# Kernel tuning notes

Hardware: AMD Instinct MI355X
Metric: run time of the kernel (lower is better)

The kernel has to match this reference:

```python
import jax, jax.numpy as jnp
import numpy as np

NUM_HEADS = 16
NUM_KV_HEADS = 4
HEAD_DIM = 64
ROPE_BASE = 10000.0


def _rope(x, pos0):
    # x: [b, s, n, h_d]; interleaved-pair RoPE (torchtune RotaryPositionalEmbeddings)
    b, s, n, hd = x.shape
    half = hd // 2
    inv_freq = 1.0 / (ROPE_BASE ** (jnp.arange(0, hd, 2, dtype=jnp.float32) / hd))  # [half]
    t = jnp.arange(s, dtype=jnp.float32) + pos0                                      # [s]
    freqs = t[:, None] * inv_freq[None, :]                                           # [s, half]
    cos = jnp.cos(freqs)[None, :, None, :].astype(x.dtype)
    sin = jnp.sin(freqs)[None, :, None, :].astype(x.dtype)
    xr = x.reshape(b, s, n, half, 2)
    x1, x2 = xr[..., 0], xr[..., 1]
    o1 = x1 * cos - x2 * sin
    o2 = x1 * sin + x2 * cos
    return jnp.stack([o1, o2], axis=-1).reshape(b, s, n, hd)


def setup_inputs() -> dict:
    key = jax.random.key(0)
    k1, k2, k3 = jax.random.split(key, 3)
    b, s, d = 2, 2048, 1024
    qkv_dim = (NUM_HEADS + 2 * NUM_KV_HEADS) * HEAD_DIM  # 1536
    x = jax.random.normal(k1, (b, s, d), dtype=jnp.float32)
    Wqkv = jax.random.normal(k2, (d, qkv_dim), dtype=jnp.float32) * (d ** -0.5)
    Wo = jax.random.normal(k3, (d, d), dtype=jnp.float32) * (d ** -0.5)
    return {"x": x, "Wqkv": Wqkv, "Wo": Wo, "curr_pos": 0}


def reference(x, Wqkv, Wo, curr_pos):
    b, s, d = x.shape
    n_h, n_kv, hd = NUM_HEADS, NUM_KV_HEADS, HEAD_DIM
    q_per_kv = n_h // n_kv
    total_qkv = q_per_kv + 2

    # fused QKV projection then split per kv group
    qkv = (x @ Wqkv).reshape(b, s, n_kv, total_qkv, hd)
    q = qkv[:, :, :, :q_per_kv]            # [b, s, n_kv, q_per_kv, hd]
    k = qkv[:, :, :, q_per_kv:q_per_kv + 1]  # [b, s, n_kv, 1, hd]
    v = qkv[:, :, :, q_per_kv + 1:]          # [b, s, n_kv, 1, hd]

    # GQA expand k/v to match query heads, then flatten heads
    k = jnp.broadcast_to(k, (b, s, n_kv, q_per_kv, hd))
    v = jnp.broadcast_to(v, (b, s, n_kv, q_per_kv, hd))
    q = q.reshape(b, s, n_h, hd)
    k = k.reshape(b, s, n_h, hd)
    v = v.reshape(b, s, n_h, hd)

    # RoPE on q and k
    q = _rope(q, curr_pos)
    k = _rope(k, curr_pos)

    # causal SDPA (kv_cache is None -> is_causal=True, mask=None, dropout=0)
    scale = 1.0 / jnp.sqrt(jnp.asarray(hd, dtype=x.dtype))
    scores = jnp.einsum('bqhd,bkhd->bhqk', q, k) * scale  # [b, n_h, s, s]
    causal = jnp.tril(jnp.ones((s, s), dtype=bool))
    scores = jnp.where(causal[None, None], scores, jnp.finfo(scores.dtype).min)
    attn = jax.nn.softmax(scores, axis=-1)
    out = jnp.einsum('bhqk,bkhd->bqhd', attn, v).reshape(b, s, n_h * hd)
    return out @ Wo
```

## Files before the change

### kernel.cpp

```cpp
#include <hip/hip_runtime.h>
#include <hip/hip_bf16.h>

typedef __attribute__((ext_vector_type(8))) short bf16x8;
typedef __attribute__((ext_vector_type(4))) short bf16x4;
typedef __attribute__((ext_vector_type(4))) float f32x4;
typedef unsigned short u16;
typedef unsigned int u32;

#define NH 16
#define NKV 4
#define HD 64
#define BB 2
#define SS 2048
#define DD 1024
#define QKVD 1536

#define QSCALE 0.18033688011112f
#define MBIAS  -12.0f

template<bool B> struct BoolC { static constexpr bool value = B; };
template<int V>  struct IntC  { static constexpr int value = V; };

__device__ __forceinline__ u16 f2b(float f){
  __hip_bfloat16 h = __float2bfloat16(f);
  u16 u; __builtin_memcpy(&u, &h, 2); return u;
}
__device__ __forceinline__ float b2f(u32 u){
  u <<= 16; float f; __builtin_memcpy(&f, &u, 4); return f;
}
__device__ __forceinline__ float exp2fast(float x){
#if __has_builtin(__builtin_amdgcn_exp2f)
  return __builtin_amdgcn_exp2f(x);
#else
  return exp2f(x);
#endif
}

__device__ __forceinline__ void gload16(const void* g, void* l){
  __builtin_amdgcn_global_load_lds((const __attribute__((address_space(1))) void*)g,
                                   (__attribute__((address_space(3))) void*)l, 16, 0, 0);
}

__device__ __forceinline__ f32x4 mfma16(bf16x4 a, bf16x4 b, f32x4 c){
#if __has_builtin(__builtin_amdgcn_mfma_f32_16x16x16bf16_1k)
  return __builtin_amdgcn_mfma_f32_16x16x16bf16_1k(a, b, c, 0, 0, 0);
#else
  asm volatile("v_mfma_f32_16x16x16_bf16 %0, %1, %2, %0" : "+v"(c) : "v"(a), "v"(b));
  return c;
#endif
}

__global__ __launch_bounds__(256) void prep1(const float* __restrict__ x,
                                             u16* __restrict__ Xb,
                                             const float* __restrict__ Wqkv,
                                             u16* __restrict__ WqkvT,
                                             const float* __restrict__ Wo,
                                             u16* __restrict__ WoT){
  __shared__ u16 tile[64][65];
  const int bid = blockIdx.x;
  if (bid < 4096){
    int idx = (bid * 256 + threadIdx.x) * 4;
    float4 v = *(const float4*)(x + idx);
    u32 lo = (u32)f2b(v.x) | ((u32)f2b(v.y) << 16);
    u32 hi = (u32)f2b(v.z) | ((u32)f2b(v.w) << 16);
    *(uint2*)(Xb + idx) = make_uint2(lo, hi);
    return;
  }
  const float* in; u16* outT; int K, N, n0, k0;
  if (bid < 4480){
    int id = bid - 4096; in = Wqkv; outT = WqkvT; K = 1024; N = 1536;
    n0 = (id % 24) * 64; k0 = (id / 24) * 64;
  } else {
    int id = bid - 4480; in = Wo; outT = WoT; K = 1024; N = 1024;
    n0 = (id % 16) * 64; k0 = (id / 16) * 64;
  }
  int cr = threadIdx.x >> 6, cc = threadIdx.x & 63;
#pragma unroll
  for (int rr = 0; rr < 16; rr++){
    int row = rr * 4 + cr;
    tile[row][cc] = f2b(in[(size_t)(k0 + row) * N + n0 + cc]);
  }
  __syncthreads();
#pragma unroll
  for (int rr = 0; rr < 16; rr++){
    int row = rr * 4 + cr;
    outT[(size_t)(n0 + row) * K + k0 + cc] = tile[cc][row];
  }
}

template<int TN, typename OT>
__global__ __launch_bounds__(256) void gemm_db(const __hip_bfloat16* __restrict__ A,
                                               const __hip_bfloat16* __restrict__ BT,
                                               OT* __restrict__ C,
                                               int M, int N, int K){
  constexpr int NW = TN / 32;
  constexpr int ABYTES = 128 * 128;
  constexpr int BBYTES = TN * 128;
  __shared__ __align__(16) char smem[2][ABYTES + BBYTES];
  const int ntn = N / TN;
  int bid = blockIdx.x;
  const int cpx = gridDim.x >> 3;
  bid = (bid & 7) * cpx + (bid >> 3);
  const int tm = bid / ntn, tn = bid % ntn;
  const int m0 = tm << 7, n0 = tn * TN;
  const int lane = threadIdx.x & 63, w = threadIdx.x >> 6;
  const int g = lane >> 4, i = lane & 15;
  const int wr = w >> 1, wc = w & 1;
  f32x4 acc[4][NW] = {};
  const int lrow = lane >> 3;
  const int lcol = ((lane & 7) ^ lrow) * 8;
  const __hip_bfloat16* ga = A  + (size_t)(m0 + w * 32 + lrow) * K + lcol;
  const __hip_bfloat16* gb = BT + (size_t)(n0 + w * 8 + lrow) * K + lcol;
  const int xr = (i & 7) << 4;

  auto stage = [&](int buf, int kt){
    char* As = smem[buf];
    char* Bs = As + ABYTES;
#pragma unroll
    for (int h = 0; h < 4; h++)
      gload16(ga + kt + (size_t)(h * 8) * K, As + w * 4096 + h * 1024);
#pragma unroll
    for (int h = 0; h < NW; h++)
      gload16(gb + kt + (size_t)(h * 32) * K, Bs + (h * 4 + w) * 1024);
  };

  stage(0, 0);
  asm volatile("s_waitcnt vmcnt(0)");
  __syncthreads();
  int cur = 0;
  for (int kt = 0; kt < K; kt += 64){
    if (kt + 64 < K) stage(cur ^ 1, kt + 64);
    const char* As = smem[cur];
    const char* Bs = As + ABYTES;
    bf16x8 af[2][4], bfr[2][NW];
#pragma unroll
    for (int kh = 0; kh < 2; kh++){
#pragma unroll
      for (int x = 0; x < 4; x++)
        af[kh][x] = *(const bf16x8*)(As + (wr * 64 + x * 16 + i) * 128 + ((kh * 64 + g * 16) ^ xr));
#pragma unroll
      for (int n = 0; n < NW; n++)
        bfr[kh][n] = *(const bf16x8*)(Bs + (wc * (TN / 2) + n * 16 + i) * 128 + ((kh * 64 + g * 16) ^ xr));
    }
    __builtin_amdgcn_s_setprio(1);
#pragma unroll
    for (int kh = 0; kh < 2; kh++)
#pragma unroll
      for (int mi = 0; mi < 4; mi++)
#pragma unroll
        for (int ni = 0; ni < NW; ni++)
          acc[mi][ni] = __builtin_amdgcn_mfma_f32_16x16x32_bf16(af[kh][mi], bfr[kh][ni], acc[mi][ni], 0, 0, 0);
    __builtin_amdgcn_s_setprio(0);
    asm volatile("s_waitcnt vmcnt(0)");
    __syncthreads();
    cur ^= 1;
  }
#pragma unroll
  for (int mi = 0; mi < 4; mi++)
#pragma unroll
    for (int ni = 0; ni < NW; ni++){
      size_t base = (size_t)(m0 + wr * 64 + mi * 16 + g * 4) * N + n0 + wc * (TN / 2) + ni * 16 + i;
#pragma unroll
      for (int r = 0; r < 4; r++){
        float v = acc[mi][ni][r];
        if constexpr (sizeof(OT) == 2) C[base + (size_t)r * N] = (OT)f2b(v);
        else                           C[base + (size_t)r * N] = v;
      }
    }
}

__global__ __launch_bounds__(256) void prep2(const u16* __restrict__ qkv,
                                             const int* __restrict__ posp,
                                             u16* __restrict__ Qr,
                                             u16* __restrict__ Kr,
                                             u16* __restrict__ Vt){
  __shared__ u16 tile[64][65];
  const int bid = blockIdx.x;
  if (bid < 10240){
    int bx = bid & 255, h20 = (bid >> 8) % 20, bi = bid / 5120;
    int t = bx * 256 + threadIdx.x;
    int p = t & 31, si = t >> 5;
    int kvh = h20 / 5, slot = h20 - kvh * 5;
    const u16* src = qkv + (size_t)(bi * SS + si) * QKVD + (kvh * 6 + slot) * 64 + 2 * p;
    u32 pair = *(const u32*)src;
    float x1 = b2f(pair & 0xffffu), x2 = b2f(pair >> 16);
    int pos0 = posp[0];
    float inv_freq = exp2fast(-(float)p * 0.4152410118609203f);
    float ang = (float)(si + pos0) * inv_freq;
    float sn, cs;
    sincosf(ang, &sn, &cs);
    float o1 = x1 * cs - x2 * sn;
    float o2 = x1 * sn + x2 * cs;
    u16* dst;
    if (slot == 4){
      dst = Kr + ((size_t)(bi * NKV + kvh) * SS + si) * 64 + 2 * p;
    } else {
      o1 *= QSCALE; o2 *= QSCALE;
      dst = Qr + ((size_t)(bi * NH + kvh * 4 + slot) * SS + si) * 64 + 2 * p;
    }
    *(u32*)dst = (u32)f2b(o1) | ((u32)f2b(o2) << 16);
    return;
  }
  int id2 = bid - 10240;
  int st0 = (id2 & 31) * 64;
  int bkv = id2 >> 5;
  int bi = bkv >> 2, kvh = bkv & 3;
  int cr = threadIdx.x >> 6, cc = threadIdx.x & 63;
  const u16* src = qkv + (size_t)(bi * SS + st0) * QKVD + (kvh * 6 + 5) * 64;
#pragma unroll
  for (int rr = 0; rr < 16; rr++){
    int row = rr * 4 + cr;
    tile[row][cc] = src[(size_t)row * QKVD + cc];
  }
  __syncthreads();
  u16* dst = Vt + (size_t)bkv * 64 * SS + st0;
#pragma unroll
  for (int rr = 0; rr < 16; rr++){
    int row = rr * 4 + cr;
    dst[(size_t)row * SS + cc] = tile[cc][row];
  }
}

__global__ __launch_bounds__(256) void attn_fwd(const __hip_bfloat16* __restrict__ Qr,
                                                const __hip_bfloat16* __restrict__ Kr,
                                                const __hip_bfloat16* __restrict__ Vt,
                                                u16* __restrict__ Ao){
  __shared__ __align__(16) char smem[32768];
  const int blk = blockIdx.x;
  const int qt = 15 - (blk >> 5);
  const int bh = blk & 31;
  const int hi = bh & 15;
  const int bi = bh >> 4;
  const int kvh = hi >> 2;
  const int lane = threadIdx.x & 63, w = threadIdx.x >> 6;
  const int g = lane >> 4, i = lane & 15;
  const int q0 = qt * 128 + w * 16;
  const u16* Qp = (const u16*)Qr + (size_t)(bi * NH + hi) * SS * 64;
  const u16* Kp = (const u16*)Kr + (size_t)(bi * NKV + kvh) * SS * 64;
  const u16* Vp = (const u16*)Vt + (size_t)(bi * NKV + kvh) * 64 * SS;
  bf16x8 qa0 = *(const bf16x8*)(Qp + (size_t)(q0 + i) * 64 + g * 8);
  bf16x8 qa1 = *(const bf16x8*)(Qp + (size_t)(q0 + i) * 64 + 32 + g * 8);
  bf16x8 qb0 = *(const bf16x8*)(Qp + (size_t)(q0 + 64 + i) * 64 + g * 8);
  bf16x8 qb1 = *(const bf16x8*)(Qp + (size_t)(q0 + 64 + i) * 64 + 32 + g * 8);

  const int srow = w * 8 + (lane >> 3);
  const int sw   = ((lane & 7) ^ (lane >> 3)) * 8;
  const int xr   = (i & 7) << 4;

  auto stage = [&](int buf, int j0){
#pragma unroll
    for (int h = 0; h < 2; h++)
      gload16(Kp + (size_t)(j0 + h * 32 + srow) * 64 + sw,
              &smem[buf * 16384 + h * 4096 + w * 1024]);
#pragma unroll
    for (int h = 0; h < 2; h++)
      gload16(Vp + (size_t)(h * 32 + srow) * SS + j0 + sw,
              &smem[buf * 16384 + 8192 + h * 4096 + w * 1024]);
  };

  float la = 0.f, lb = 0.f;
  f32x4 oa[4] = {}, ob[4] = {};
  const int wlim = w * 16 + i;

  auto body = [&](auto modec, int buf){
    constexpr int MODE = decltype(modec)::value;
    const char* Kb = &smem[buf * 16384];
    const char* Vb = Kb + 8192;
    f32x4 sta[4], stb[4];
    __builtin_amdgcn_s_setprio(1);
#pragma unroll
    for (int jb = 0; jb < 4; jb++){
      const int row = jb * 16 + i;
      bf16x8 kf0 = *(const bf16x8*)(Kb + row * 128 + ((g * 16) ^ xr));
      bf16x8 kf1 = *(const bf16x8*)(Kb + row * 128 + ((64 + g * 16) ^ xr));
      if constexpr (MODE != 2){
        f32x4 a = {MBIAS, MBIAS, MBIAS, MBIAS};
        a = __builtin_amdgcn_mfma_f32_16x16x32_bf16(kf0, qa0, a, 0, 0, 0);
        a = __builtin_amdgcn_mfma_f32_16x16x32_bf16(kf1, qa1, a, 0, 0, 0);
        sta[jb] = a;
      }
      f32x4 b = {MBIAS, MBIAS, MBIAS, MBIAS};
      b = __builtin_amdgcn_mfma_f32_16x16x32_bf16(kf0, qb0, b, 0, 0, 0);
      b = __builtin_amdgcn_mfma_f32_16x16x32_bf16(kf1, qb1, b, 0, 0, 0);
      stb[jb] = b;
    }
    __builtin_amdgcn_s_setprio(0);
    bf16x4 vt[4][4];
#pragma unroll
    for (int db = 0; db < 4; db++){
      const int row = db * 16 + i;
#pragma unroll
      for (int mk = 0; mk < 4; mk++)
        vt[db][mk] = *(const bf16x4*)(Vb + row * 128 + ((mk * 32 + g * 8) ^ xr));
    }
    auto smpv = [&](auto diagc, f32x4* st, f32x4* o, float& l){
      constexpr bool DIAG = decltype(diagc)::value;
      float p[4][4];
#pragma unroll
      for (int jb = 0; jb < 4; jb++)
#pragma unroll
        for (int r = 0; r < 4; r++){
          float e = exp2fast(st[jb][r]);
          if constexpr (DIAG) e = (jb * 16 + g * 4 + r > wlim) ? 0.f : e;
          p[jb][r] = e;
        }
      float sj[4];
#pragma unroll
      for (int jb = 0; jb < 4; jb++)
        sj[jb] = (p[jb][0] + p[jb][1]) + (p[jb][2] + p[jb][3]);
      float lsum = (sj[0] + sj[1]) + (sj[2] + sj[3]);
      lsum += __shfl_xor(lsum, 16, 64);
      lsum += __shfl_xor(lsum, 32, 64);
      l += lsum;
      __builtin_amdgcn_s_setprio(1);
#pragma unroll
      for (int mk = 0; mk < 4; mk++){
        bf16x4 pa;
#pragma unroll
        for (int r = 0; r < 4; r++) pa[r] = (short)f2b(p[mk][r]);
#pragma unroll
        for (int db = 0; db < 4; db++)
          o[db] = mfma16(vt[db][mk], pa, o[db]);
      }
      __builtin_amdgcn_s_setprio(0);
    };
    if constexpr (MODE == 0){
      smpv(BoolC<false>{}, sta, oa, la);
      smpv(BoolC<false>{}, stb, ob, lb);
    } else if constexpr (MODE == 1){
      smpv(BoolC<true>{},  sta, oa, la);
      smpv(BoolC<false>{}, stb, ob, lb);
    } else {
      smpv(BoolC<true>{},  stb, ob, lb);
    }
  };

  stage(0, 0);
  asm volatile("s_waitcnt vmcnt(0)");
  __syncthreads();
  int cur = 0;
  const int nfull = 2 * qt;
  for (int kt = 0; kt < nfull; kt++){
    stage(cur ^ 1, (kt + 1) * 64);
    body(IntC<0>{}, cur);
    asm volatile("s_waitcnt vmcnt(0)");
    __syncthreads();
    cur ^= 1;
  }
  stage(cur ^ 1, (nfull + 1) * 64);
  body(IntC<1>{}, cur);
  asm volatile("s_waitcnt vmcnt(0)");
  __syncthreads();
  cur ^= 1;
  body(IntC<2>{}, cur);

  const float linva = 1.f / la;
  const float linvb = 1.f / lb;
  u16* orowa = Ao + (size_t)(bi * SS + q0 + i) * (NH * HD) + hi * 64 + g * 4;
  u16* orowb = orowa + (size_t)64 * (NH * HD);
#pragma unroll
  for (int db = 0; db < 4; db++){
    bf16x4 ova, ovb;
#pragma unroll
    for (int r = 0; r < 4; r++){
      ova[r] = (short)f2b(oa[db][r] * linva);
      ovb[r] = (short)f2b(ob[db][r] * linvb);
    }
    *(bf16x4*)(orowa + db * 16) = ova;
    *(bf16x4*)(orowb + db * 16) = ovb;
  }
}

extern "C" void kernel_launch(void* const* d_in, const int* in_sizes, int n_in,
                              void* d_out, int out_size, void* d_ws, size_t ws_size,
                              hipStream_t stream){
  const float* x    = (const float*)d_in[0];
  const float* Wqkv = (const float*)d_in[1];
  const float* Wo   = (const float*)d_in[2];
  const int*   pos  = (const int*)d_in[3];
  float* out = (float*)d_out;
  char* ws = (char*)d_ws;

  __hip_bfloat16* Xb    = (__hip_bfloat16*)(ws);
  __hip_bfloat16* WqkvT = (__hip_bfloat16*)(ws + 8388608);
  __hip_bfloat16* WoT   = (__hip_bfloat16*)(ws + 11534336);
  u16*            QKVb  = (u16*)(ws + 13631488);
  __hip_bfloat16* Qr    = (__hip_bfloat16*)(ws + 26214400);
  __hip_bfloat16* Kr    = (__hip_bfloat16*)(ws + 34603008);
  __hip_bfloat16* Vt    = (__hip_bfloat16*)(ws + 36700160);
  __hip_bfloat16* Ao    = (__hip_bfloat16*)(ws);

  prep1<<<4736, 256, 0, stream>>>(x, (u16*)Xb, Wqkv, (u16*)WqkvT, Wo, (u16*)WoT);
  gemm_db<96, u16><<<512, 256, 0, stream>>>(Xb, WqkvT, QKVb, 4096, 1536, 1024);
  prep2<<<10496, 256, 0, stream>>>(QKVb, pos, (u16*)Qr, (u16*)Kr, (u16*)Vt);
  attn_fwd<<<512, 256, 0, stream>>>(Qr, Kr, Vt, (u16*)Ao);
  gemm_db<64, float><<<512, 256, 0, stream>>>(Ao, WoT, out, 4096, 1024, 1024);
}
```

Measured before the change: 94.03 us.

## Split attention block across eight waves with one query tile per wave

The attention kernel now launches 512 threads per block. Each of the eight waves owns a single 16-row query tile, where previously each of four waves handled two tiles 64 rows apart. K/V staging is spread across all eight waves with one 16-byte load each, and the diagonal and last-tile masking is specialised per wave, so waves 0-3 skip the final tile. The intent is more waves per CU to hide latency and lower per-wave register pressure. The cost is more synchronisation participants per barrier and idle waves during the final masked step.

```diff
diff --git a/kernel.cpp b/kernel.cpp
--- a/kernel.cpp
+++ b/kernel.cpp
@@ -221,7 +221,7 @@
   }
 }
 
-__global__ __launch_bounds__(256) void attn_fwd(const __hip_bfloat16* __restrict__ Qr,
+__global__ __launch_bounds__(512) void attn_fwd(const __hip_bfloat16* __restrict__ Qr,
                                                 const __hip_bfloat16* __restrict__ Kr,
                                                 const __hip_bfloat16* __restrict__ Vt,
                                                 u16* __restrict__ Ao){
@@ -232,57 +232,45 @@
   const int hi = bh & 15;
   const int bi = bh >> 4;
   const int kvh = hi >> 2;
-  const int lane = threadIdx.x & 63, w = threadIdx.x >> 6;
+  const int tid = threadIdx.x;
+  const int lane = tid & 63, w = tid >> 6;
   const int g = lane >> 4, i = lane & 15;
   const int q0 = qt * 128 + w * 16;
   const u16* Qp = (const u16*)Qr + (size_t)(bi * NH + hi) * SS * 64;
   const u16* Kp = (const u16*)Kr + (size_t)(bi * NKV + kvh) * SS * 64;
   const u16* Vp = (const u16*)Vt + (size_t)(bi * NKV + kvh) * 64 * SS;
-  bf16x8 qa0 = *(const bf16x8*)(Qp + (size_t)(q0 + i) * 64 + g * 8);
-  bf16x8 qa1 = *(const bf16x8*)(Qp + (size_t)(q0 + i) * 64 + 32 + g * 8);
-  bf16x8 qb0 = *(const bf16x8*)(Qp + (size_t)(q0 + 64 + i) * 64 + g * 8);
-  bf16x8 qb1 = *(const bf16x8*)(Qp + (size_t)(q0 + 64 + i) * 64 + 32 + g * 8);
-
-  const int srow = w * 8 + (lane >> 3);
-  const int sw   = ((lane & 7) ^ (lane >> 3)) * 8;
+  bf16x8 qf0 = *(const bf16x8*)(Qp + (size_t)(q0 + i) * 64 + g * 8);
+  bf16x8 qf1 = *(const bf16x8*)(Qp + (size_t)(q0 + i) * 64 + 32 + g * 8);
+
+  const int srow = tid >> 3;
+  const int sw   = ((tid & 7) ^ (srow & 7)) * 8;
   const int xr   = (i & 7) << 4;
 
   auto stage = [&](int buf, int j0){
-#pragma unroll
-    for (int h = 0; h < 2; h++)
-      gload16(Kp + (size_t)(j0 + h * 32 + srow) * 64 + sw,
-              &smem[buf * 16384 + h * 4096 + w * 1024]);
-#pragma unroll
-    for (int h = 0; h < 2; h++)
-      gload16(Vp + (size_t)(h * 32 + srow) * SS + j0 + sw,
-              &smem[buf * 16384 + 8192 + h * 4096 + w * 1024]);
+    gload16(Kp + (size_t)(j0 + srow) * 64 + sw, &smem[buf * 16384 + w * 1024]);
+    gload16(Vp + (size_t)srow * SS + j0 + sw,   &smem[buf * 16384 + 8192 + w * 1024]);
   };
 
-  float la = 0.f, lb = 0.f;
-  f32x4 oa[4] = {}, ob[4] = {};
+  float l_row = 0.f;
+  f32x4 o[4] = {};
   const int wlim = w * 16 + i;
 
   auto body = [&](auto modec, int buf){
     constexpr int MODE = decltype(modec)::value;
+    if constexpr (MODE == 2){ if (w < 4) return; }
     const char* Kb = &smem[buf * 16384];
     const char* Vb = Kb + 8192;
-    f32x4 sta[4], stb[4];
+    f32x4 st[4];
     __builtin_amdgcn_s_setprio(1);
 #pragma unroll
     for (int jb = 0; jb < 4; jb++){
       const int row = jb * 16 + i;
       bf16x8 kf0 = *(const bf16x8*)(Kb + row * 128 + ((g * 16) ^ xr));
       bf16x8 kf1 = *(const bf16x8*)(Kb + row * 128 + ((64 + g * 16) ^ xr));
-      if constexpr (MODE != 2){
-        f32x4 a = {MBIAS, MBIAS, MBIAS, MBIAS};
-        a = __builtin_amdgcn_mfma_f32_16x16x32_bf16(kf0, qa0, a, 0, 0, 0);
-        a = __builtin_amdgcn_mfma_f32_16x16x32_bf16(kf1, qa1, a, 0, 0, 0);
-        sta[jb] = a;
-      }
-      f32x4 b = {MBIAS, MBIAS, MBIAS, MBIAS};
-      b = __builtin_amdgcn_mfma_f32_16x16x32_bf16(kf0, qb0, b, 0, 0, 0);
-      b = __builtin_amdgcn_mfma_f32_16x16x32_bf16(kf1, qb1, b, 0, 0, 0);
-      stb[jb] = b;
+      f32x4 a = {MBIAS, MBIAS, MBIAS, MBIAS};
+      a = __builtin_amdgcn_mfma_f32_16x16x32_bf16(kf0, qf0, a, 0, 0, 0);
+      a = __builtin_amdgcn_mfma_f32_16x16x32_bf16(kf1, qf1, a, 0, 0, 0);
+      st[jb] = a;
     }
     __builtin_amdgcn_s_setprio(0);
     bf16x4 vt[4][4];
@@ -293,7 +281,7 @@
       for (int mk = 0; mk < 4; mk++)
         vt[db][mk] = *(const bf16x4*)(Vb + row * 128 + ((mk * 32 + g * 8) ^ xr));
     }
-    auto smpv = [&](auto diagc, f32x4* st, f32x4* o, float& l){
+    auto smpv = [&](auto diagc, int wl){
       constexpr bool DIAG = decltype(diagc)::value;
       float p[4][4];
 #pragma unroll
@@ -301,7 +289,7 @@
 #pragma unroll
         for (int r = 0; r < 4; r++){
           float e = exp2fast(st[jb][r]);
-          if constexpr (DIAG) e = (jb * 16 + g * 4 + r > wlim) ? 0.f : e;
+          if constexpr (DIAG) e = (jb * 16 + g * 4 + r > wl) ? 0.f : e;
           p[jb][r] = e;
         }
       float sj[4];
@@ -311,7 +299,7 @@
       float lsum = (sj[0] + sj[1]) + (sj[2] + sj[3]);
       lsum += __shfl_xor(lsum, 16, 64);
       lsum += __shfl_xor(lsum, 32, 64);
-      l += lsum;
+      l_row += lsum;
       __builtin_amdgcn_s_setprio(1);
 #pragma unroll
       for (int mk = 0; mk < 4; mk++){
@@ -325,13 +313,12 @@
       __builtin_amdgcn_s_setprio(0);
     };
     if constexpr (MODE == 0){
-      smpv(BoolC<false>{}, sta, oa, la);
-      smpv(BoolC<false>{}, stb, ob, lb);
+      smpv(BoolC<false>{}, 0);
     } else if constexpr (MODE == 1){
-      smpv(BoolC<true>{},  sta, oa, la);
-      smpv(BoolC<false>{}, stb, ob, lb);
+      if (w < 4) smpv(BoolC<true>{}, wlim);
+      else       smpv(BoolC<false>{}, 0);
     } else {
-      smpv(BoolC<true>{},  stb, ob, lb);
+      smpv(BoolC<true>{}, wlim - 64);
     }
   };
 
@@ -354,20 +341,14 @@
   cur ^= 1;
   body(IntC<2>{}, cur);
 
-  const float linva = 1.f / la;
-  const float linvb = 1.f / lb;
-  u16* orowa = Ao + (size_t)(bi * SS + q0 + i) * (NH * HD) + hi * 64 + g * 4;
-  u16* orowb = orowa + (size_t)64 * (NH * HD);
+  const float linv = 1.f / l_row;
+  u16* orow = Ao + (size_t)(bi * SS + q0 + i) * (NH * HD) + hi * 64 + g * 4;
 #pragma unroll
   for (int db = 0; db < 4; db++){
-    bf16x4 ova, ovb;
-#pragma unroll
-    for (int r = 0; r < 4; r++){
-      ova[r] = (short)f2b(oa[db][r] * linva);
-      ovb[r] = (short)f2b(ob[db][r] * linvb);
-    }
-    *(bf16x4*)(orowa + db * 16) = ova;
-    *(bf16x4*)(orowb + db * 16) = ovb;
+    bf16x4 ov;
+#pragma unroll
+    for (int r = 0; r < 4; r++) ov[r] = (short)f2b(o[db][r] * linv);
+    *(bf16x4*)(orow + db * 16) = ov;
   }
 }
 
@@ -393,6 +374,6 @@
   prep1<<<4736, 256, 0, stream>>>(x, (u16*)Xb, Wqkv, (u16*)WqkvT, Wo, (u16*)WoT);
   gemm_db<96, u16><<<512, 256, 0, stream>>>(Xb, WqkvT, QKVb, 4096, 1536, 1024);
   prep2<<<10496, 256, 0, stream>>>(QKVb, pos, (u16*)Qr, (u16*)Kr, (u16*)Vt);
-  attn_fwd<<<512, 256, 0, stream>>>(Qr, Kr, Vt, (u16*)Ao);
+  attn_fwd<<<512, 512, 0, stream>>>(Qr, Kr, Vt, (u16*)Ao);
   gemm_db<64, float><<<512, 256, 0, stream>>>(Ao, WoT, out, 4096, 1024, 1024);
 }
```

Measured after the change: 91.47 us. 2.7% less time.
